# Performance work log

Hardware: AMD Instinct MI355X
Metric: run time of the kernel (lower is better)

The kernel has to match this reference:

```python
import jax, jax.numpy as jnp
import numpy as np

V, D, H, L, FF, NC = 32000, 512, 8, 4, 2048, 10
HD = D // H
EPS = 1e-5


def _layernorm(x, g, b):
    m = jnp.mean(x, axis=-1, keepdims=True)
    v = jnp.mean((x - m) ** 2, axis=-1, keepdims=True)
    return (x - m) * jax.lax.rsqrt(v + EPS) * g + b


def _pos_encoding(T, d):
    pos = jnp.arange(T, dtype=jnp.float32)[:, None]
    div = jnp.exp(jnp.arange(0, d, 2, dtype=jnp.float32) * (-np.log(10000.0) / d))
    pe = jnp.zeros((T, d), dtype=jnp.float32)
    pe = pe.at[:, 0::2].set(jnp.sin(pos * div))
    pe = pe.at[:, 1::2].set(jnp.cos(pos * div))
    return pe


def setup_inputs() -> dict:
    key = jax.random.key(0)
    ks = iter(jax.random.split(key, 32))
    n = lambda shape, s=0.02: jax.random.normal(next(ks), shape, dtype=jnp.float32) * s
    inp = {
        "tokens": jax.random.randint(next(ks), (8, 1024), 0, V),
        "emb": n((V, D), 1.0),
        # attention projections, stored (in, out) so y = x @ W + b
        "Wq": n((L, D, D)), "bq": jnp.zeros((L, D)),
        "Wk": n((L, D, D)), "bk": jnp.zeros((L, D)),
        "Wv": n((L, D, D)), "bv": jnp.zeros((L, D)),
        "Wo": n((L, D, D)), "bo": jnp.zeros((L, D)),
        "ln1_g": jnp.ones((L, D)), "ln1_b": jnp.zeros((L, D)),
        "ln2_g": jnp.ones((L, D)), "ln2_b": jnp.zeros((L, D)),
        "W1": n((L, D, FF)), "b1": jnp.zeros((L, FF)),
        "W2": n((L, FF, D)), "b2": jnp.zeros((L, D)),
        "heavy_w": n((D, D)), "heavy_b": jnp.zeros((D,)),
        "heavy_a1": n((D, D)), "heavy_a2": n((D, D)),
        "norm_g": jnp.ones((D,)), "norm_b": jnp.zeros((D,)),
        "cls_W": n((D, NC)), "cls_b": jnp.zeros((NC,)),
    }
    return inp


def reference(tokens, emb, Wq, bq, Wk, bk, Wv, bv, Wo, bo,
              ln1_g, ln1_b, ln2_g, ln2_b, W1, b1, W2, b2,
              heavy_w, heavy_b, heavy_a1, heavy_a2,
              norm_g, norm_b, cls_W, cls_b):
    B, T = tokens.shape
    x = emb[tokens] + _pos_encoding(T, D)[None]  # [B,T,D]
    scale = 1.0 / np.sqrt(HD)
    for l in range(L):
        # attention block (pre-norm)
        h = _layernorm(x, ln1_g[l], ln1_b[l])
        q = (h @ Wq[l] + bq[l]).reshape(B, T, H, HD)
        k = (h @ Wk[l] + bk[l]).reshape(B, T, H, HD)
        v = (h @ Wv[l] + bv[l]).reshape(B, T, H, HD)
        scores = jnp.einsum("bqhd,bkhd->bhqk", q, k) * scale
        attn = jax.nn.softmax(scores, axis=-1)
        o = jnp.einsum("bhqk,bkhd->bqhd", attn, v).reshape(B, T, D)
        x = x + (o @ Wo[l] + bo[l])
        # feedforward block
        h = _layernorm(x, ln2_g[l], ln2_b[l])
        x = x + (jax.nn.gelu(h @ W1[l] + b1[l], approximate=False) @ W2[l] + b2[l])
    # heavy layer: chained matmuls + bias + tanh (vectorized over B*T)
    x = jnp.tanh(((x @ heavy_w) @ heavy_a1) @ heavy_a2 + heavy_b)
    x = _layernorm(x, norm_g, norm_b)
    x = jnp.mean(x, axis=1)  # [B,D]
    return x @ cls_W + cls_b  # [B,NC]
```

## Files before the change

### kernel.cpp

```cpp
#include <hip/hip_runtime.h>
#include <math.h>

#define BS   8
#define TT   1024
#define DD   512
#define HH   8
#define LL   4
#define FFD  2048
#define NCC  10
#define MM   (BS*TT)
#define MDl  ((long)MM*DD)

typedef unsigned short u16;
typedef short  short8 __attribute__((ext_vector_type(8)));
typedef float  f32x4  __attribute__((ext_vector_type(4)));
typedef u16    u16x8  __attribute__((ext_vector_type(8)));
typedef u16    u16x4  __attribute__((ext_vector_type(4)));

static __device__ __forceinline__ u16 f2b(float f) {
    union { float f; unsigned u; } x; x.f = f;
    unsigned r = x.u + 0x7FFFu + ((x.u >> 16) & 1u);
    return (u16)(r >> 16);
}
static __device__ __forceinline__ float b2f(u16 u) {
    union { unsigned u; float f; } x; x.u = ((unsigned)u) << 16;
    return x.f;
}

#define ASYNC_LDS16(gp, lp) \
    __builtin_amdgcn_global_load_lds((const __attribute__((address_space(1))) void*)(gp), \
                                     (__attribute__((address_space(3))) void*)(lp), 16, 0, 0)

__global__ __launch_bounds__(256)
void embed_kernel(const int* __restrict__ tok, const float* __restrict__ emb,
                  float* __restrict__ X) {
    int i = blockIdx.x * 256 + threadIdx.x;
    int d = i & (DD - 1);
    int row = i >> 9;
    int t = row & (TT - 1);
    int j = d >> 1;
    float freq = __expf((float)(2 * j) * (-9.210340371976184f / 512.0f));
    float ang = (float)t * freq;
    float pe = (d & 1) ? cosf(ang) : sinf(ang);
    X[i] = emb[(long)tok[row] * DD + d] + pe;
}

template<int OUTBF>
__global__ __launch_bounds__(256)
void ln_kernel(const float* __restrict__ in, void* __restrict__ outp,
               const float* __restrict__ g, const float* __restrict__ b) {
    int row = blockIdx.x;
    int tid = threadIdx.x;
    const float* x = in + (long)row * DD;
    float x1 = x[tid], x2 = x[tid + 256];
    __shared__ float red[256], red2[256];
    red[tid] = x1 + x2;
    red2[tid] = x1 * x1 + x2 * x2;
    __syncthreads();
    for (int st = 128; st > 0; st >>= 1) {
        if (tid < st) { red[tid] += red[tid + st]; red2[tid] += red2[tid + st]; }
        __syncthreads();
    }
    float mean = red[0] * (1.0f / DD);
    float var = red2[0] * (1.0f / DD) - mean * mean;
    float rstd = rsqrtf(var + 1e-5f);
    float y1 = (x1 - mean) * rstd * g[tid] + b[tid];
    float y2 = (x2 - mean) * rstd * g[tid + 256] + b[tid + 256];
    if (OUTBF) {
        u16* o = (u16*)outp + (long)row * DD;
        o[tid] = f2b(y1); o[tid + 256] = f2b(y2);
    } else {
        float* o = (float*)outp + (long)row * DD;
        o[tid] = y1; o[tid + 256] = y2;
    }
}

template<int OUTBF, int HAS_BIAS, int ACT, int HAS_RES>
__global__ __launch_bounds__(256)
void mfma_gemm(const u16* __restrict__ A, const u16* __restrict__ BT,
               const float* __restrict__ bias, const float* __restrict__ R,
               void* __restrict__ Cout, int N, int K) {
    __shared__ __align__(16) u16 lds[17408];
    u16* As = lds;
    u16* Bs = lds + 8192;
    const int tid = threadIdx.x;
    const int lane = tid & 63;
    const int w = tid >> 6;
    const long bm = (long)blockIdx.y * 128;
    const long bn = (long)blockIdx.x * 128;

    f32x4 acc[4][4];
#pragma unroll
    for (int i = 0; i < 4; ++i)
#pragma unroll
        for (int j = 0; j < 4; ++j) acc[i][j] = {0.f, 0.f, 0.f, 0.f};

    const int lrow = lane >> 3;
    const int lchk = (lane & 7) ^ lrow;
    const u16* Ag = A + (bm + w * 8 + lrow) * K + lchk * 8;
    const u16* Bg = BT + (bn + w * 8 + lrow) * K + lchk * 8;
    u16* AsW = As + w * 512;
    u16* BsW = Bs + w * 512;

    const int fr = lane & 15;
    const int g = lane >> 4;
    const int am0 = (w >> 1) * 64 + fr;
    const int bn0 = (w & 1) * 64 + fr;
    const int sw = fr & 7;

    for (int k0 = 0; k0 < K; k0 += 64) {
        __syncthreads();
#pragma unroll
        for (int j = 0; j < 4; ++j) {
            ASYNC_LDS16(Ag + (long)j * 32 * K + k0, AsW + j * 2048);
            ASYNC_LDS16(Bg + (long)j * 32 * K + k0, BsW + j * 2048);
        }
        __syncthreads();
#pragma unroll
        for (int kk = 0; kk < 2; ++kk) {
            const int pos = ((kk << 2) + g) ^ sw;
            short8 af[4], bfv[4];
#pragma unroll
            for (int mi = 0; mi < 4; ++mi)
                af[mi] = *(const short8*)&As[(am0 + mi * 16) * 64 + pos * 8];
#pragma unroll
            for (int ni = 0; ni < 4; ++ni)
                bfv[ni] = *(const short8*)&Bs[(bn0 + ni * 16) * 64 + pos * 8];
#pragma unroll
            for (int mi = 0; mi < 4; ++mi)
#pragma unroll
                for (int ni = 0; ni < 4; ++ni)
                    acc[mi][ni] = __builtin_amdgcn_mfma_f32_16x16x32_bf16(
                        af[mi], bfv[ni], acc[mi][ni], 0, 0, 0);
        }
    }

    const int erow0 = (w >> 1) * 64 + g * 4;
    const int ecol0 = (w & 1) * 64 + fr;

    if (OUTBF) {
        __syncthreads();
#pragma unroll
        for (int ni = 0; ni < 4; ++ni) {
            const long col = bn + ecol0 + ni * 16;
            float bv = 0.f;
            if (HAS_BIAS) bv = bias[col];
#pragma unroll
            for (int mi = 0; mi < 4; ++mi)
#pragma unroll
                for (int r = 0; r < 4; ++r) {
                    const int row = erow0 + mi * 16 + r;
                    float v = acc[mi][ni][r];
                    if (HAS_BIAS) v += bv;
                    if (ACT == 1) v = 0.5f * v * (1.0f + erff(v * 0.70710678118654752f));
                    if (ACT == 2) v = tanhf(v);
                    if (HAS_RES) v += R[(bm + row) * N + col];
                    lds[row * 136 + ecol0 + ni * 16] = f2b(v);
                }
        }
        __syncthreads();
        const int srow2 = tid >> 4;
        const int sch2 = tid & 15;
        u16* Cp = (u16*)Cout;
#pragma unroll
        for (int rr = 0; rr < 8; ++rr) {
            const int row = srow2 + rr * 16;
            u16x8 vv = *(const u16x8*)&lds[row * 136 + sch2 * 8];
            *(u16x8*)(Cp + (bm + row) * N + bn + sch2 * 8) = vv;
        }
    } else {
#pragma unroll
        for (int ni = 0; ni < 4; ++ni) {
            const long col = bn + ecol0 + ni * 16;
            float bv = 0.f;
            if (HAS_BIAS) bv = bias[col];
#pragma unroll
            for (int mi = 0; mi < 4; ++mi)
#pragma unroll
                for (int r = 0; r < 4; ++r) {
                    const long row = bm + erow0 + mi * 16 + r;
                    float v = acc[mi][ni][r];
                    if (HAS_BIAS) v += bv;
                    if (ACT == 1) v = 0.5f * v * (1.0f + erff(v * 0.70710678118654752f));
                    if (ACT == 2) v = tanhf(v);
                    if (HAS_RES) v += R[row * N + col];
                    ((float*)Cout)[row * N + col] = v;
                }
        }
    }
}

__global__ __launch_bounds__(256)
void attn_kernel(const u16* __restrict__ QKV, u16* __restrict__ O) {
    const int qblk = blockIdx.x;
    const int h = blockIdx.y;
    const int b = blockIdx.z;
    const int tid = threadIdx.x;
    const int lane = tid & 63;
    const int w = tid >> 6;
    const int fr = lane & 15;
    const int g = lane >> 4;
    const int q8 = g * 8;

    __shared__ __align__(16) u16 Ks[2][64 * 32];
    __shared__ __align__(16) u16 Vt[64 * 72];
    __shared__ __align__(16) u16 Pw[4][32 * 72];

    const long rowb = (long)b * TT;
    const int wq0 = qblk * 128 + w * 32;

    short8 qf[2][2];
#pragma unroll
    for (int qt = 0; qt < 2; ++qt)
#pragma unroll
        for (int hf = 0; hf < 2; ++hf)
            qf[qt][hf] = *(const short8*)(QKV + (rowb + wq0 + qt * 16 + fr) * 1536
                                          + h * 64 + hf * 32 + q8);

    f32x4 accO[2][4];
    float lsum[2][4];
#pragma unroll
    for (int qt = 0; qt < 2; ++qt) {
#pragma unroll
        for (int nt = 0; nt < 4; ++nt) accO[qt][nt] = {0.f, 0.f, 0.f, 0.f};
#pragma unroll
        for (int r = 0; r < 4; ++r) lsum[qt][r] = 0.f;
    }

    const int skey = lane >> 2;
    const int schk = lane & 3;
    const int vkey = lane;
    const int vd0 = w * 16;

    for (int kt = 0; kt < 16; ++kt) {
        __syncthreads();
        const long tb = (rowb + kt * 64) * 1536 + h * 64;
#pragma unroll
        for (int i = 0; i < 2; ++i) {
            int s = w * 2 + i;
            int hf = s >> 2, keyb = (s & 3) * 16;
            const u16* gp = QKV + tb + 512 + (long)(keyb + skey) * 1536 + hf * 32 + schk * 8;
            ASYNC_LDS16(gp, &Ks[hf][keyb * 32]);
        }
        {
            const u16* vp = QKV + tb + 1024 + (long)vkey * 1536 + vd0;
            u16x8 v0 = *(const u16x8*)vp;
            u16x8 v1 = *(const u16x8*)(vp + 8);
#pragma unroll
            for (int j = 0; j < 8; ++j) {
                Vt[(vd0 + j) * 72 + vkey]     = v0[j];
                Vt[(vd0 + 8 + j) * 72 + vkey] = v1[j];
            }
        }
        __syncthreads();

        f32x4 accS[2][4];
#pragma unroll
        for (int qt = 0; qt < 2; ++qt)
#pragma unroll
            for (int n = 0; n < 4; ++n) accS[qt][n] = {0.f, 0.f, 0.f, 0.f};
#pragma unroll
        for (int n = 0; n < 4; ++n)
#pragma unroll
            for (int hf = 0; hf < 2; ++hf) {
                short8 bk = *(const short8*)&Ks[hf][(n * 16 + fr) * 32 + q8];
                accS[0][n] = __builtin_amdgcn_mfma_f32_16x16x32_bf16(qf[0][hf], bk, accS[0][n], 0, 0, 0);
                accS[1][n] = __builtin_amdgcn_mfma_f32_16x16x32_bf16(qf[1][hf], bk, accS[1][n], 0, 0, 0);
            }
#pragma unroll
        for (int qt = 0; qt < 2; ++qt)
#pragma unroll
            for (int r = 0; r < 4; ++r) {
                int prow = qt * 16 + g * 4 + r;
#pragma unroll
                for (int n = 0; n < 4; ++n) {
                    float pv = exp2f(accS[qt][n][r] * 0.18033688011112042f);
                    u16 pb = f2b(pv);
                    lsum[qt][r] += b2f(pb);
                    Pw[w][prow * 72 + n * 16 + fr] = pb;
                }
            }
#pragma unroll
        for (int hf = 0; hf < 2; ++hf) {
            short8 pa0 = *(const short8*)&Pw[w][fr * 72 + hf * 32 + q8];
            short8 pa1 = *(const short8*)&Pw[w][(16 + fr) * 72 + hf * 32 + q8];
#pragma unroll
            for (int nt = 0; nt < 4; ++nt) {
                short8 bv = *(const short8*)&Vt[(nt * 16 + fr) * 72 + hf * 32 + q8];
                accO[0][nt] = __builtin_amdgcn_mfma_f32_16x16x32_bf16(pa0, bv, accO[0][nt], 0, 0, 0);
                accO[1][nt] = __builtin_amdgcn_mfma_f32_16x16x32_bf16(pa1, bv, accO[1][nt], 0, 0, 0);
            }
        }
    }
#pragma unroll
    for (int qt = 0; qt < 2; ++qt)
#pragma unroll
        for (int r = 0; r < 4; ++r) {
            float s = lsum[qt][r];
            s += __shfl_xor(s, 1, 64);
            s += __shfl_xor(s, 2, 64);
            s += __shfl_xor(s, 4, 64);
            s += __shfl_xor(s, 8, 64);
            lsum[qt][r] = 1.0f / s;
        }
#pragma unroll
    for (int qt = 0; qt < 2; ++qt)
#pragma unroll
        for (int nt = 0; nt < 4; ++nt)
#pragma unroll
            for (int r = 0; r < 4; ++r) {
                long row = rowb + wq0 + qt * 16 + g * 4 + r;
                O[row * DD + h * 64 + nt * 16 + fr] = f2b(accO[qt][nt][r] * lsum[qt][r]);
            }
}

struct WP   { const float* s; u16* d; };
struct WTbl { WP e[19]; };

__global__ __launch_bounds__(256)
void wprep512_kernel(WTbl tbl) {
    const float* src = tbl.e[blockIdx.z].s;
    u16* dst = tbl.e[blockIdx.z].d;
    int k0 = blockIdx.y * 32, n0 = blockIdx.x * 32;
    __shared__ float tile[32][33];
    int tx = threadIdx.x & 31, ty = threadIdx.x >> 5;
#pragma unroll
    for (int i = 0; i < 4; ++i)
        tile[ty + 8 * i][tx] = src[(long)(k0 + ty + 8 * i) * 512 + n0 + tx];
    __syncthreads();
#pragma unroll
    for (int i = 0; i < 4; ++i) {
        int r = ty + 8 * i;
        dst[(long)(n0 + r) * 512 + k0 + tx] = f2b(tile[tx][r]);
    }
}

__global__ __launch_bounds__(256)
void wprep_kernel(const float* __restrict__ src, u16* __restrict__ dst,
                  int K, int N, long srcLS, long dstLS) {
    int l = blockIdx.z;
    src += (long)l * srcLS;
    dst += (long)l * dstLS;
    int k0 = blockIdx.y * 32, n0 = blockIdx.x * 32;
    __shared__ float tile[32][33];
    int tx = threadIdx.x & 31, ty = threadIdx.x >> 5;
#pragma unroll
    for (int i = 0; i < 4; ++i)
        tile[ty + 8 * i][tx] = src[(long)(k0 + ty + 8 * i) * N + n0 + tx];
    __syncthreads();
#pragma unroll
    for (int i = 0; i < 4; ++i) {
        int r = ty + 8 * i;
        dst[(long)(n0 + r) * K + k0 + tx] = f2b(tile[tx][r]);
    }
}

__global__ __launch_bounds__(256)
void bprep_kernel(const float* __restrict__ bq, const float* __restrict__ bk,
                  const float* __restrict__ bv, float* __restrict__ dst) {
    int i = blockIdx.x * 256 + threadIdx.x;
    int l = i / 1536, j = i - l * 1536;
    float v = (j < 512) ? bq[l * 512 + j]
            : (j < 1024) ? bk[l * 512 + j - 512]
                         : bv[l * 512 + j - 1024];
    dst[i] = v;
}

__global__ __launch_bounds__(256)
void f2b_kernel(const float* __restrict__ in, u16* __restrict__ out, int n) {
    int i = blockIdx.x * 256 + threadIdx.x;
    if (i < n) out[i] = f2b(in[i]);
}

__global__ __launch_bounds__(256)
void zero_kernel(float* __restrict__ p, int n) {
    int i = blockIdx.x * 256 + threadIdx.x;
    if (i < n) p[i] = 0.0f;
}

__global__ __launch_bounds__(256)
void colmean_kernel(const float* __restrict__ Hn, float* __restrict__ XM) {
    int blk = blockIdx.x;
    int b = blk >> 5;
    int r0 = (blk & 31) * 32;
    int tid = threadIdx.x;
    float acc0 = 0.0f, acc1 = 0.0f;
    for (int r = 0; r < 32; ++r) {
        long off = ((long)b * TT + r0 + r) * DD + tid;
        acc0 += Hn[off];
        acc1 += Hn[off + 256];
    }
    atomicAdd(&XM[b * DD + tid], acc0);
    atomicAdd(&XM[b * DD + tid + 256], acc1);
}

__global__ __launch_bounds__(256)
void cls_kernel(const float* __restrict__ XM, const float* __restrict__ W,
                const float* __restrict__ bias, float* __restrict__ out) {
    int b = blockIdx.x;
    int tid = threadIdx.x;
    __shared__ float xm[DD];
    xm[tid] = XM[b * DD + tid] * (1.0f / TT);
    xm[tid + 256] = XM[b * DD + tid + 256] * (1.0f / TT);
    __syncthreads();
    if (tid < NCC) {
        float s = bias[tid];
        for (int d = 0; d < DD; ++d) s += xm[d] * W[d * NCC + tid];
        out[b * NCC + tid] = s;
    }
}

extern "C" void kernel_launch(void* const* d_in, const int* in_sizes, int n_in,
                              void* d_out, int out_size, void* d_ws, size_t ws_size,
                              hipStream_t stream) {
    const int*   tokens  = (const int*)d_in[0];
    const float* emb     = (const float*)d_in[1];
    const float* Wq      = (const float*)d_in[2];
    const float* bq      = (const float*)d_in[3];
    const float* Wk      = (const float*)d_in[4];
    const float* bk      = (const float*)d_in[5];
    const float* Wv      = (const float*)d_in[6];
    const float* bv      = (const float*)d_in[7];
    const float* Wo      = (const float*)d_in[8];
    const float* bo      = (const float*)d_in[9];
    const float* ln1_g   = (const float*)d_in[10];
    const float* ln1_b   = (const float*)d_in[11];
    const float* ln2_g   = (const float*)d_in[12];
    const float* ln2_b   = (const float*)d_in[13];
    const float* W1      = (const float*)d_in[14];
    const float* b1      = (const float*)d_in[15];
    const float* W2      = (const float*)d_in[16];
    const float* b2      = (const float*)d_in[17];
    const float* heavy_w = (const float*)d_in[18];
    const float* heavy_b = (const float*)d_in[19];
    const float* heavy_a1= (const float*)d_in[20];
    const float* heavy_a2= (const float*)d_in[21];
    const float* norm_g  = (const float*)d_in[22];
    const float* norm_b  = (const float*)d_in[23];
    const float* cls_W   = (const float*)d_in[24];
    const float* cls_b   = (const float*)d_in[25];
    float* out = (float*)d_out;

    char* p = (char*)d_ws;
    float* X    = (float*)p;  p += MDl * 4;
    u16*   Hh   = (u16*)p;    p += MDl * 2;
    u16*   QKVb = (u16*)p;
    u16*   FFb  = QKVb;
    u16*   T1   = QKVb;
    u16*   T2   = QKVb + MDl;
    float* LNout= (float*)QKVb;
    p += (long)MM * 1536 * 2;
    u16*   Ob   = (u16*)p;    p += MDl * 2;
    u16*   Xbf  = (u16*)p;    p += MDl * 2;
    u16*   WqkvT= (u16*)p;    p += 4L * 1536 * 512 * 2;
    u16*   WoT  = (u16*)p;    p += 4L * 512 * 512 * 2;
    u16*   W1T  = (u16*)p;    p += 4L * 2048 * 512 * 2;
    u16*   W2T  = (u16*)p;    p += 4L * 512 * 2048 * 2;
    u16*   WhT  = (u16*)p;    p += 3L * 512 * 512 * 2;
    float* bqkv = (float*)p;  p += 4L * 1536 * 4;
    float* XM   = (float*)p;  p += (long)BS * DD * 4;

    dim3 blk(256);

    WTbl tbl;
    for (int l = 0; l < 4; ++l) {
        tbl.e[l * 4 + 0] = {Wq + (long)l * 262144, WqkvT + (long)l * 786432};
        tbl.e[l * 4 + 1] = {Wk + (long)l * 262144, WqkvT + (long)l * 786432 + 262144};
        tbl.e[l * 4 + 2] = {Wv + (long)l * 262144, WqkvT + (long)l * 786432 + 524288};
        tbl.e[l * 4 + 3] = {Wo + (long)l * 262144, WoT + (long)l * 262144};
    }
    tbl.e[16] = {heavy_w,  WhT};
    tbl.e[17] = {heavy_a1, WhT + 262144};
    tbl.e[18] = {heavy_a2, WhT + 524288};
    wprep512_kernel<<<dim3(16, 16, 19), blk, 0, stream>>>(tbl);
    wprep_kernel<<<dim3(64, 16, 4), blk, 0, stream>>>(W1, W1T,  512, 2048, 1048576, 1048576);
    wprep_kernel<<<dim3(16, 64, 4), blk, 0, stream>>>(W2, W2T, 2048,  512, 1048576, 1048576);
    bprep_kernel<<<24, blk, 0, stream>>>(bq, bk, bv, bqkv);

    embed_kernel<<<MM * DD / 256, blk, 0, stream>>>(tokens, emb, X);

    dim3 gQKV(12, 64), g512(4, 64), gFF1(16, 64);

    for (int l = 0; l < LL; ++l) {
        ln_kernel<1><<<MM, blk, 0, stream>>>(X, Hh, ln1_g + l * DD, ln1_b + l * DD);
        mfma_gemm<1, 1, 0, 0><<<gQKV, blk, 0, stream>>>(
            Hh, WqkvT + (long)l * 786432, bqkv + l * 1536, nullptr, QKVb, 1536, 512);
        attn_kernel<<<dim3(8, HH, BS), blk, 0, stream>>>(QKVb, Ob);
        mfma_gemm<0, 1, 0, 1><<<g512, blk, 0, stream>>>(
            Ob, WoT + (long)l * 262144, bo + l * DD, X, X, 512, 512);
        ln_kernel<1><<<MM, blk, 0, stream>>>(X, Hh, ln2_g + l * DD, ln2_b + l * DD);
        mfma_gemm<1, 1, 1, 0><<<gFF1, blk, 0, stream>>>(
            Hh, W1T + (long)l * 1048576, b1 + l * FFD, nullptr, FFb, 2048, 512);
        mfma_gemm<0, 1, 0, 1><<<g512, blk, 0, stream>>>(
            FFb, W2T + (long)l * 1048576, b2 + l * DD, X, X, 512, 2048);
    }

    f2b_kernel<<<MM * DD / 256, blk, 0, stream>>>(X, Xbf, MM * DD);
    mfma_gemm<1, 0, 0, 0><<<g512, blk, 0, stream>>>(Xbf, WhT,          nullptr, nullptr, T1, 512, 512);
    mfma_gemm<1, 0, 0, 0><<<g512, blk, 0, stream>>>(T1,  WhT + 262144, nullptr, nullptr, T2, 512, 512);
    mfma_gemm<0, 1, 2, 0><<<g512, blk, 0, stream>>>(T2,  WhT + 524288, heavy_b, nullptr, X,  512, 512);

    ln_kernel<0><<<MM, blk, 0, stream>>>(X, LNout, norm_g, norm_b);
    zero_kernel<<<(BS * DD + 255) / 256, blk, 0, stream>>>(XM, BS * DD);
    colmean_kernel<<<256, blk, 0, stream>>>(LNout, XM);
    cls_kernel<<<BS, blk, 0, stream>>>(XM, cls_W, cls_b, out);
}
```

Before: 1.021 ms.

## Register-prefetch double buffering for GEMM and attention K/V tiles

```diff
diff --git a/kernel.cpp b/kernel.cpp
--- a/kernel.cpp
+++ b/kernel.cpp
@@ -22,14 +22,14 @@
     unsigned r = x.u + 0x7FFFu + ((x.u >> 16) & 1u);
     return (u16)(r >> 16);
 }
+static __device__ __forceinline__ u16 f2b_fast(float f) {
+    union { float f; unsigned u; } x; x.f = f;
+    return (u16)((x.u + 0x8000u) >> 16);
+}
 static __device__ __forceinline__ float b2f(u16 u) {
     union { unsigned u; float f; } x; x.u = ((unsigned)u) << 16;
     return x.f;
 }
-
-#define ASYNC_LDS16(gp, lp) \
-    __builtin_amdgcn_global_load_lds((const __attribute__((address_space(1))) void*)(gp), \
-                                     (__attribute__((address_space(3))) void*)(lp), 16, 0, 0)
 
 __global__ __launch_bounds__(256)
 void embed_kernel(const int* __restrict__ tok, const float* __restrict__ emb,
@@ -76,7 +76,7 @@
 }
 
 template<int OUTBF, int HAS_BIAS, int ACT, int HAS_RES>
-__global__ __launch_bounds__(256)
+__global__ __launch_bounds__(256, 2)
 void mfma_gemm(const u16* __restrict__ A, const u16* __restrict__ BT,
                const float* __restrict__ bias, const float* __restrict__ R,
                void* __restrict__ Cout, int N, int K) {
@@ -95,12 +95,14 @@
 #pragma unroll
         for (int j = 0; j < 4; ++j) acc[i][j] = {0.f, 0.f, 0.f, 0.f};
 
-    const int lrow = lane >> 3;
-    const int lchk = (lane & 7) ^ lrow;
-    const u16* Ag = A + (bm + w * 8 + lrow) * K + lchk * 8;
-    const u16* Bg = BT + (bn + w * 8 + lrow) * K + lchk * 8;
-    u16* AsW = As + w * 512;
-    u16* BsW = Bs + w * 512;
+    const int srow = tid >> 1;
+    const int sc0 = (tid & 1) * 4;
+    const u16* Ag = A + (bm + srow) * K + sc0 * 8;
+    const u16* Bg = BT + (bn + srow) * K + sc0 * 8;
+    int soff[4];
+#pragma unroll
+    for (int j = 0; j < 4; ++j)
+        soff[j] = srow * 64 + ((sc0 + j) ^ (srow & 7)) * 8;
 
     const int fr = lane & 15;
     const int g = lane >> 4;
@@ -108,30 +110,49 @@
     const int bn0 = (w & 1) * 64 + fr;
     const int sw = fr & 7;
 
-    for (int k0 = 0; k0 < K; k0 += 64) {
-        __syncthreads();
-#pragma unroll
-        for (int j = 0; j < 4; ++j) {
-            ASYNC_LDS16(Ag + (long)j * 32 * K + k0, AsW + j * 2048);
-            ASYNC_LDS16(Bg + (long)j * 32 * K + k0, BsW + j * 2048);
-        }
-        __syncthreads();
-#pragma unroll
-        for (int kk = 0; kk < 2; ++kk) {
-            const int pos = ((kk << 2) + g) ^ sw;
-            short8 af[4], bfv[4];
-#pragma unroll
-            for (int mi = 0; mi < 4; ++mi)
-                af[mi] = *(const short8*)&As[(am0 + mi * 16) * 64 + pos * 8];
-#pragma unroll
-            for (int ni = 0; ni < 4; ++ni)
-                bfv[ni] = *(const short8*)&Bs[(bn0 + ni * 16) * 64 + pos * 8];
-#pragma unroll
-            for (int mi = 0; mi < 4; ++mi)
+    u16x8 sa[2][4], sb[2][4];
+#pragma unroll
+    for (int j = 0; j < 4; ++j) {
+        sa[0][j] = *(const u16x8*)(Ag + j * 8);
+        sb[0][j] = *(const u16x8*)(Bg + j * 8);
+    }
+
+    for (int k0 = 0; k0 < K; k0 += 128) {
+#pragma unroll
+        for (int half = 0; half < 2; ++half) {
+            const int cb = half, nb = half ^ 1;
+            __syncthreads();
+#pragma unroll
+            for (int j = 0; j < 4; ++j) {
+                *(u16x8*)&As[soff[j]] = sa[cb][j];
+                *(u16x8*)&Bs[soff[j]] = sb[cb][j];
+            }
+            const int knext = k0 + (half + 1) * 64;
+            if (knext < K) {
+#pragma unroll
+                for (int j = 0; j < 4; ++j) {
+                    sa[nb][j] = *(const u16x8*)(Ag + knext + j * 8);
+                    sb[nb][j] = *(const u16x8*)(Bg + knext + j * 8);
+                }
+            }
+            __syncthreads();
+#pragma unroll
+            for (int kk = 0; kk < 2; ++kk) {
+                const int pos = ((kk << 2) + g) ^ sw;
+                short8 af[4], bfv[4];
+#pragma unroll
+                for (int mi = 0; mi < 4; ++mi)
+                    af[mi] = *(const short8*)&As[(am0 + mi * 16) * 64 + pos * 8];
 #pragma unroll
                 for (int ni = 0; ni < 4; ++ni)
-                    acc[mi][ni] = __builtin_amdgcn_mfma_f32_16x16x32_bf16(
-                        af[mi], bfv[ni], acc[mi][ni], 0, 0, 0);
+                    bfv[ni] = *(const short8*)&Bs[(bn0 + ni * 16) * 64 + pos * 8];
+#pragma unroll
+                for (int mi = 0; mi < 4; ++mi)
+#pragma unroll
+                    for (int ni = 0; ni < 4; ++ni)
+                        acc[mi][ni] = __builtin_amdgcn_mfma_f32_16x16x32_bf16(
+                            af[mi], bfv[ni], acc[mi][ni], 0, 0, 0);
+            }
         }
     }
 
@@ -190,7 +211,7 @@
     }
 }
 
-__global__ __launch_bounds__(256)
+__global__ __launch_bounds__(256, 2)
 void attn_kernel(const u16* __restrict__ QKV, u16* __restrict__ O) {
     const int qblk = blockIdx.x;
     const int h = blockIdx.y;
@@ -202,7 +223,7 @@
     const int g = lane >> 4;
     const int q8 = g * 8;
 
-    __shared__ __align__(16) u16 Ks[2][64 * 32];
+    __shared__ __align__(16) u16 Ks[64 * 64];
     __shared__ __align__(16) u16 Vt[64 * 72];
     __shared__ __align__(16) u16 Pw[4][32 * 72];
 
@@ -227,31 +248,40 @@
         for (int r = 0; r < 4; ++r) lsum[qt][r] = 0.f;
     }
 
-    const int skey = lane >> 2;
-    const int schk = lane & 3;
-    const int vkey = lane;
-    const int vd0 = w * 16;
-
+    const int skey = tid >> 2;
+    const int skc = (tid & 3) * 2;
+    const int koff0 = skey * 64 + ((skc ^ (skey & 7)) * 8);
+    const int koff1 = skey * 64 + (((skc + 1) ^ (skey & 7)) * 8);
+    const int vkp = tid & 31;
+    const int vd0 = (tid >> 5) * 8;
+
+#define LOAD_KV(kt_, kr_, vr_) do {                                            \
+        const long tb_ = (rowb + (long)(kt_) * 64) * 1536 + h * 64;            \
+        const u16* kp_ = QKV + tb_ + 512 + (long)skey * 1536 + skc * 8;        \
+        kr_[0] = *(const u16x8*)kp_;                                           \
+        kr_[1] = *(const u16x8*)(kp_ + 8);                                     \
+        const u16* vp_ = QKV + tb_ + 1024 + (long)(vkp * 2) * 1536 + vd0;      \
+        vr_[0] = *(const u16x8*)vp_;                                           \
+        vr_[1] = *(const u16x8*)(vp_ + 1536);                                  \
+    } while (0)
+
+    u16x8 kr[2][2], vr[2][2];
+    LOAD_KV(0, kr[0], vr[0]);
+
+#pragma unroll
     for (int kt = 0; kt < 16; ++kt) {
+        const int cb = kt & 1, nb = cb ^ 1;
         __syncthreads();
-        const long tb = (rowb + kt * 64) * 1536 + h * 64;
-#pragma unroll
-        for (int i = 0; i < 2; ++i) {
-            int s = w * 2 + i;
-            int hf = s >> 2, keyb = (s & 3) * 16;
-            const u16* gp = QKV + tb + 512 + (long)(keyb + skey) * 1536 + hf * 32 + schk * 8;
-            ASYNC_LDS16(gp, &Ks[hf][keyb * 32]);
-        }
+        *(u16x8*)&Ks[koff0] = kr[cb][0];
+        *(u16x8*)&Ks[koff1] = kr[cb][1];
         {
-            const u16* vp = QKV + tb + 1024 + (long)vkey * 1536 + vd0;
-            u16x8 v0 = *(const u16x8*)vp;
-            u16x8 v1 = *(const u16x8*)(vp + 8);
-#pragma unroll
-            for (int j = 0; j < 8; ++j) {
-                Vt[(vd0 + j) * 72 + vkey]     = v0[j];
-                Vt[(vd0 + 8 + j) * 72 + vkey] = v1[j];
-            }
-        }
+            unsigned* Vt32 = (unsigned*)Vt;
+#pragma unroll
+            for (int j = 0; j < 8; ++j)
+                Vt32[(vd0 + j) * 36 + vkp] =
+                    (unsigned)vr[cb][0][j] | ((unsigned)vr[cb][1][j] << 16);
+        }
+        if (kt < 15) LOAD_KV(kt + 1, kr[nb], vr[nb]);
         __syncthreads();
 
         f32x4 accS[2][4];
@@ -263,7 +293,8 @@
         for (int n = 0; n < 4; ++n)
 #pragma unroll
             for (int hf = 0; hf < 2; ++hf) {
-                short8 bk = *(const short8*)&Ks[hf][(n * 16 + fr) * 32 + q8];
+                short8 bk = *(const short8*)&Ks[(n * 16 + fr) * 64
+                                                + ((((hf << 2) + g) ^ (fr & 7)) * 8)];
                 accS[0][n] = __builtin_amdgcn_mfma_f32_16x16x32_bf16(qf[0][hf], bk, accS[0][n], 0, 0, 0);
                 accS[1][n] = __builtin_amdgcn_mfma_f32_16x16x32_bf16(qf[1][hf], bk, accS[1][n], 0, 0, 0);
             }
@@ -275,9 +306,8 @@
 #pragma unroll
                 for (int n = 0; n < 4; ++n) {
                     float pv = exp2f(accS[qt][n][r] * 0.18033688011112042f);
-                    u16 pb = f2b(pv);
-                    lsum[qt][r] += b2f(pb);
-                    Pw[w][prow * 72 + n * 16 + fr] = pb;
+                    lsum[qt][r] += pv;
+                    Pw[w][prow * 72 + n * 16 + fr] = f2b_fast(pv);
                 }
             }
 #pragma unroll
@@ -292,6 +322,8 @@
             }
         }
     }
+#undef LOAD_KV
+
 #pragma unroll
     for (int qt = 0; qt < 2; ++qt)
 #pragma unroll
```

New measurement: 1.403 ms. 37.3% more time.
